# Kernel optimization log

Measured on AMD Instinct MI355X. Metric: run time of the kernel, lower is better.

The kernel has to match this reference:

```python
import jax, jax.numpy as jnp
import numpy as np

D = 1024      # hidden_size
FF = 4096     # ff_inner_dim = 4 * D
E = 8         # num_experts
K = 2         # moe_top_k
B, L = 4, 1024


def setup_inputs() -> dict:
    key = jax.random.key(0)
    ks = jax.random.split(key, 12)
    s = 0.02  # weight init scale
    return {
        "x": jax.random.normal(ks[0], (B, L, D), jnp.float32),
        "W_gate": jax.random.normal(ks[1], (D, E), jnp.float32) * s,
        "W1": jax.random.normal(ks[2], (E, D, FF), jnp.float32) * s,
        "b1": jnp.zeros((E, FF), jnp.float32),
        "W2": jax.random.normal(ks[3], (E, FF, D), jnp.float32) * s,
        "b2": jnp.zeros((E, D), jnp.float32),
        "Ws1": jax.random.normal(ks[4], (D, FF), jnp.float32) * s,
        "bs1": jnp.zeros((FF,), jnp.float32),
        "Ws2": jax.random.normal(ks[5], (FF, D), jnp.float32) * s,
        "bs2": jnp.zeros((D,), jnp.float32),
    }


def _gelu(h):
    # torch F.gelu default = exact (erf) gelu
    return jax.nn.gelu(h, approximate=False)


def reference(x, W_gate, W1, b1, W2, b2, Ws1, bs1, Ws2, bs2):
    Bx, Lx, Dx = x.shape
    xf = x.reshape(-1, Dx)                       # [T, D]
    logits = xf @ W_gate                         # [T, E]
    probs = jax.nn.softmax(logits, axis=-1)
    top_v, top_i = jax.lax.top_k(probs, K)       # [T, K]
    top_v = top_v / jnp.sum(top_v, axis=-1, keepdims=True)
    # dense combine weights: [T, E], zero for unselected experts
    combine = jnp.sum(jax.nn.one_hot(top_i, E, dtype=xf.dtype) * top_v[..., None], axis=1)

    out = jnp.zeros_like(xf)
    for e in range(E):  # fixed small expert loop, unrolled under jit
        h = _gelu(xf @ W1[e] + b1[e])            # [T, FF]
        out = out + combine[:, e:e + 1] * (h @ W2[e] + b2[e])

    shared = _gelu(xf @ Ws1 + bs1) @ Ws2 + bs2   # [T, D]
    return (out + shared).reshape(Bx, Lx, Dx)
```

## Files before the change

### kernel.cpp

```cpp
#include <hip/hip_runtime.h>
#include <hip/hip_bf16.h>

typedef unsigned short ushort_t;
typedef __attribute__((ext_vector_type(4))) float f32x4;
typedef __attribute__((ext_vector_type(8))) short bf16x8;
typedef __attribute__((ext_vector_type(8))) unsigned short us8;

#define T_TOK 4096
#define D_DIM 1024
#define FF_DIM 4096
#define NE 8
#define ESTRIDE 4194304L

__device__ __forceinline__ unsigned short f2bf(float f) {
  __hip_bfloat16 h = __float2bfloat16(f);
  return __builtin_bit_cast(unsigned short, h);
}
__device__ __forceinline__ float gelu_f(float v) {
  return 0.5f * v * (1.0f + erff(v * 0.70710678118654752440f));
}

__global__ void gate_kernel(const float* __restrict__ x, const float* __restrict__ Wg,
                            int* __restrict__ cnt, int* __restrict__ tok,
                            float* __restrict__ wof, int* __restrict__ rankof) {
  const int t = blockIdx.x;
  const int lane = threadIdx.x;
  const float* xr = x + (long)t * D_DIM;
  float acc[NE];
#pragma unroll
  for (int e = 0; e < NE; e++) acc[e] = 0.f;
#pragma unroll
  for (int i = 0; i < 16; i++) {
    int d = i * 64 + lane;
    float xv = xr[d];
    const float* wr = Wg + d * NE;
#pragma unroll
    for (int e = 0; e < NE; e++) acc[e] += xv * wr[e];
  }
#pragma unroll
  for (int off = 32; off > 0; off >>= 1) {
#pragma unroll
    for (int e = 0; e < NE; e++) acc[e] += __shfl_xor(acc[e], off, 64);
  }
  if (lane == 0) {
    int i0 = 0;
#pragma unroll
    for (int e = 1; e < NE; e++) if (acc[e] > acc[i0]) i0 = e;
    int i1 = -1;
#pragma unroll
    for (int e = 0; e < NE; e++) {
      if (e == i0) continue;
      if (i1 < 0 || acc[e] > acc[i1]) i1 = e;
    }
    float e1 = expf(acc[i1] - acc[i0]);
    float w0 = 1.f / (1.f + e1);
    float w1 = e1 * w0;
    int s0 = atomicAdd(&cnt[i0], 1);
    tok[i0 * T_TOK + s0] = t; wof[i0 * T_TOK + s0] = w0; rankof[i0 * T_TOK + s0] = 0;
    int s1 = atomicAdd(&cnt[i1], 1);
    tok[i1 * T_TOK + s1] = t; wof[i1 * T_TOK + s1] = w1; rankof[i1 * T_TOK + s1] = 1;
    tok[8 * T_TOK + t] = t; wof[8 * T_TOK + t] = 1.f; rankof[8 * T_TOK + t] = 0;
  }
}

__global__ void scan_kernel(int* cnt, int* base) {
  if (threadIdx.x == 0 && blockIdx.x == 0) {
    int s = 0;
    for (int e = 0; e < NE; e++) { base[e] = s; s += cnt[e]; }
    base[8] = s;
    cnt[8] = T_TOK;
  }
}

__global__ void cvt_x_kernel(const float* __restrict__ src, ushort_t* __restrict__ dst) {
  long i = ((long)blockIdx.x * 256 + threadIdx.x) * 8;
  float4 v0 = *(const float4*)(src + i);
  float4 v1 = *(const float4*)(src + i + 4);
  us8 o;
  o[0] = f2bf(v0.x); o[1] = f2bf(v0.y); o[2] = f2bf(v0.z); o[3] = f2bf(v0.w);
  o[4] = f2bf(v1.x); o[5] = f2bf(v1.y); o[6] = f2bf(v1.z); o[7] = f2bf(v1.w);
  *(us8*)(dst + i) = o;
}

__global__ void tcvt_kernel(const float* __restrict__ src, ushort_t* __restrict__ dst,
                            int R, int C) {
  src += (long)blockIdx.z * R * C;
  dst += (long)blockIdx.z * R * C;
  const int r0 = blockIdx.y * 64, c0 = blockIdx.x * 64;
  __shared__ ushort_t tile[64][72];
  const int t = threadIdx.x;
#pragma unroll
  for (int i = 0; i < 4; i++) {
    int lin = t + i * 256;
    int r = lin >> 4;
    int c = (lin & 15) * 4;
    float4 v = *(const float4*)(src + (long)(r0 + r) * C + c0 + c);
    tile[c + 0][r] = f2bf(v.x);
    tile[c + 1][r] = f2bf(v.y);
    tile[c + 2][r] = f2bf(v.z);
    tile[c + 3][r] = f2bf(v.w);
  }
  __syncthreads();
#pragma unroll
  for (int i = 0; i < 2; i++) {
    int lin = t + i * 256;
    int cc = lin >> 3, rp = lin & 7;
    us8 v = *(const us8*)&tile[cc][rp * 8];
    *(us8*)(dst + (long)(c0 + cc) * R + r0 + rp * 8) = v;
  }
}

template <int K, int N, int PHASE>
__global__ __launch_bounds__(512, 2) void gemm_kernel(
    const ushort_t* __restrict__ Abase, const ushort_t* __restrict__ WT,
    const float* __restrict__ bias_e, const float* __restrict__ bias_s,
    const int* __restrict__ cnt, const int* __restrict__ base,
    const int* __restrict__ tok, const float* __restrict__ wof,
    const int* __restrict__ rankof,
    ushort_t* __restrict__ He, float* __restrict__ ybuf, float* __restrict__ out) {
  const int e = blockIdx.z;
  const int count = cnt[e];
  const int m0 = blockIdx.y * 256;
  if (m0 >= count) return;
  const int n0 = blockIdx.x * 256;
  const int tid = threadIdx.x;
  const int w = tid >> 6, lane = tid & 63;
  const int wm = w >> 2, wn = w & 3;
  const int lr = lane & 15, lg = lane >> 4;

  __shared__ ushort_t lds_u[16 * 4096];
  char* const lds = (char*)lds_u;

  constexpr int NT = K / 32;

  const int srow = tid >> 2;
  const int kcg = (tid & 3) ^ ((tid >> 3) & 3);
  const ushort_t* bsrc[4];
#pragma unroll
  for (int c = 0; c < 2; c++) {
    int rr = m0 + c * 128 + srow;
    int rc = (rr < count) ? rr : 0;
    long arow;
    if (PHASE == 1) arow = tok[e * T_TOK + rc];
    else            arow = (long)base[e] + rc;
    bsrc[c] = Abase + arow * (long)K + kcg * 8;
  }
#pragma unroll
  for (int c = 0; c < 2; c++) {
    long brow = n0 + c * 128 + srow;
    bsrc[2 + c] = WT + (long)e * ESTRIDE + brow * (long)K + kcg * 8;
  }

#define STAGE(g_, c_, tg_)                                                     \
  __builtin_amdgcn_global_load_lds(                                            \
      (const __attribute__((address_space(1))) void*)(bsrc[c_] + (long)(tg_) * 32), \
      (__attribute__((address_space(3))) void*)(lds + ((g_) & 15) * 8192 + w * 1024), \
      16, 0, 0)

  int offA[8], offB[4];
#pragma unroll
  for (int m = 0; m < 8; m++) {
    int r = m * 16 + lr;
    offA[m] = r * 64 + ((lg ^ ((r >> 1) & 3)) << 4);
  }
#pragma unroll
  for (int n = 0; n < 4; n++) {
    int r = (wn & 1) * 64 + n * 16 + lr;
    offB[n] = r * 64 + ((lg ^ ((r >> 1) & 3)) << 4);
  }

  f32x4 acc[8][4] = {};

#pragma unroll
  for (int g = 0; g < 8; g++) STAGE(g, g & 3, g >> 2);

  int sA = wm;
  int sB = 2 + (wn >> 1);

  for (int t = 0; t < NT; t++) {
    if (t == NT - 1) { asm volatile("s_waitcnt vmcnt(0)" ::: "memory"); }
    else             { asm volatile("s_waitcnt vmcnt(4)" ::: "memory"); }
    __builtin_amdgcn_s_barrier();
    asm volatile("" ::: "memory");

    const char* pa = lds + sA * 8192;
    const char* pb = lds + sB * 8192;

    if (t + 2 < NT) { STAGE(4 * t + 8, 0, t + 2); STAGE(4 * t + 9, 1, t + 2); }
    bf16x8 av[8];
#pragma unroll
    for (int m = 0; m < 8; m++) av[m] = *(const bf16x8*)(pa + offA[m]);
    bf16x8 bv0 = *(const bf16x8*)(pb + offB[0]);
    bf16x8 bv1 = *(const bf16x8*)(pb + offB[1]);
    __builtin_amdgcn_s_setprio(1);
#pragma unroll
    for (int m = 0; m < 8; m++) {
      acc[m][0] = __builtin_amdgcn_mfma_f32_16x16x32_bf16(av[m], bv0, acc[m][0], 0, 0, 0);
      acc[m][1] = __builtin_amdgcn_mfma_f32_16x16x32_bf16(av[m], bv1, acc[m][1], 0, 0, 0);
    }
    __builtin_amdgcn_s_setprio(0);

    if (t + 2 < NT) { STAGE(4 * t + 10, 2, t + 2); STAGE(4 * t + 11, 3, t + 2); }
    bf16x8 bv2 = *(const bf16x8*)(pb + offB[2]);
    bf16x8 bv3 = *(const bf16x8*)(pb + offB[3]);
    __builtin_amdgcn_s_setprio(1);
#pragma unroll
    for (int m = 0; m < 8; m++) {
      acc[m][2] = __builtin_amdgcn_mfma_f32_16x16x32_bf16(av[m], bv2, acc[m][2], 0, 0, 0);
      acc[m][3] = __builtin_amdgcn_mfma_f32_16x16x32_bf16(av[m], bv3, acc[m][3], 0, 0, 0);
    }
    __builtin_amdgcn_s_setprio(0);

    sA = (sA + 4) & 15;
    sB = (sB + 4) & 15;
  }
#undef STAGE

  const float* bias = (e == NE) ? bias_s : (bias_e + (long)e * N);
#pragma unroll
  for (int m = 0; m < 8; m++) {
#pragma unroll
    for (int j = 0; j < 4; j++) {
      int rloc = wm * 128 + m * 16 + lg * 4 + j;
      int rr = m0 + rloc;
      if (rr >= count) continue;
      if (PHASE == 1) {
        long orow = (long)base[e] + rr;
#pragma unroll
        for (int n = 0; n < 4; n++) {
          int col = n0 + wn * 64 + n * 16 + lr;
          float v = acc[m][n][j] + bias[col];
          He[orow * FF_DIM + col] = f2bf(gelu_f(v));
        }
      } else {
        int tt = tok[e * T_TOK + rr];
        if (e == NE) {
#pragma unroll
          for (int n = 0; n < 4; n++) {
            int col = n0 + wn * 64 + n * 16 + lr;
            out[(long)tt * D_DIM + col] = acc[m][n][j] + bias[col];
          }
        } else {
          float wgt = wof[e * T_TOK + rr];
          int rk = rankof[e * T_TOK + rr];
          float* dst = ybuf + (long)rk * ((long)T_TOK * D_DIM) + (long)tt * D_DIM;
#pragma unroll
          for (int n = 0; n < 4; n++) {
            int col = n0 + wn * 64 + n * 16 + lr;
            dst[col] = wgt * (acc[m][n][j] + bias[col]);
          }
        }
      }
    }
  }
}

__global__ void final_add_kernel(float* __restrict__ out, const float* __restrict__ ybuf) {
  long i = ((long)blockIdx.x * 256 + threadIdx.x) * 4;
  float4 a = *(const float4*)(out + i);
  float4 b = *(const float4*)(ybuf + i);
  float4 c = *(const float4*)(ybuf + (long)T_TOK * D_DIM + i);
  a.x += b.x + c.x; a.y += b.y + c.y; a.z += b.z + c.z; a.w += b.w + c.w;
  *(float4*)(out + i) = a;
}

extern "C" void kernel_launch(void* const* d_in, const int* in_sizes, int n_in,
                              void* d_out, int out_size, void* d_ws, size_t ws_size,
                              hipStream_t stream) {
  (void)in_sizes; (void)n_in; (void)out_size; (void)ws_size;
  const float* x   = (const float*)d_in[0];
  const float* Wg  = (const float*)d_in[1];
  const float* W1  = (const float*)d_in[2];
  const float* b1  = (const float*)d_in[3];
  const float* W2  = (const float*)d_in[4];
  const float* b2  = (const float*)d_in[5];
  const float* Ws1 = (const float*)d_in[6];
  const float* bs1 = (const float*)d_in[7];
  const float* Ws2 = (const float*)d_in[8];
  const float* bs2 = (const float*)d_in[9];
  float* out = (float*)d_out;

  char* ws = (char*)d_ws;
  int*      cnt    = (int*)(ws + 0);
  int*      base   = (int*)(ws + 64);
  int*      tok    = (int*)(ws + 256);
  float*    wof    = (float*)(ws + 256 + 147456);
  int*      rankof = (int*)(ws + 256 + 2 * 147456);
  ushort_t* Xbf    = (ushort_t*)(ws + 442624);
  ushort_t* W1T    = (ushort_t*)(ws + 8831232);
  ushort_t* W2T    = (ushort_t*)(ws + 84328704);
  ushort_t* He     = (ushort_t*)(ws + 159826176);
  float*    ybuf   = (float*)(ws + 261538048);

  hipMemsetAsync(cnt, 0, 64, stream);
  gate_kernel<<<T_TOK, 64, 0, stream>>>(x, Wg, cnt, tok, wof, rankof);
  scan_kernel<<<1, 64, 0, stream>>>(cnt, base);
  cvt_x_kernel<<<2048, 256, 0, stream>>>(x, Xbf);
  tcvt_kernel<<<dim3(64, 16, 8), 256, 0, stream>>>(W1, W1T, 1024, 4096);
  tcvt_kernel<<<dim3(16, 64, 8), 256, 0, stream>>>(W2, W2T, 4096, 1024);
  tcvt_kernel<<<dim3(64, 16, 1), 256, 0, stream>>>(Ws1, W1T + 8L * ESTRIDE, 1024, 4096);
  tcvt_kernel<<<dim3(16, 64, 1), 256, 0, stream>>>(Ws2, W2T + 8L * ESTRIDE, 4096, 1024);
  gemm_kernel<1024, 4096, 1><<<dim3(16, 16, 9), 512, 0, stream>>>(
      Xbf, W1T, b1, bs1, cnt, base, tok, wof, rankof, He, ybuf, out);
  gemm_kernel<4096, 1024, 2><<<dim3(4, 16, 9), 512, 0, stream>>>(
      He, W2T, b2, bs2, cnt, base, tok, wof, rankof, He, ybuf, out);
  final_add_kernel<<<4096, 256, 0, stream>>>(out, ybuf);
}
```

Baseline: 627.3 us.

## Restructure MoE GEMM main loop into 4-phase ping-pong with K=64 tiles

New measurement: 625.9 us. Within noise of the previous version (-0.2%).

```diff
diff --git a/kernel.cpp b/kernel.cpp
--- a/kernel.cpp
+++ b/kernel.cpp
@@ -127,94 +127,141 @@
   const int w = tid >> 6, lane = tid & 63;
   const int wm = w >> 2, wn = w & 3;
   const int lr = lane & 15, lg = lane >> 4;
-
-  __shared__ ushort_t lds_u[16 * 4096];
+  const int swk = ((lg ^ ((lr >> 1) & 3)) << 4);
+
+  __shared__ ushort_t lds_u[2 * 32768];
   char* const lds = (char*)lds_u;
 
-  constexpr int NT = K / 32;
-
-  const int srow = tid >> 2;
-  const int kcg = (tid & 3) ^ ((tid >> 3) & 3);
-  const ushort_t* bsrc[4];
-#pragma unroll
-  for (int c = 0; c < 2; c++) {
-    int rr = m0 + c * 128 + srow;
+  constexpr int NT = K / 64;
+
+  const int sr2 = tid >> 2;
+  const int kc2 = (tid & 3) ^ ((tid >> 3) & 3);
+  const ushort_t* pA[2];
+  const ushort_t* pB[2];
+#pragma unroll
+  for (int h = 0; h < 2; h++) {
+    int rr = m0 + h * 128 + sr2;
     int rc = (rr < count) ? rr : 0;
     long arow;
     if (PHASE == 1) arow = tok[e * T_TOK + rc];
     else            arow = (long)base[e] + rc;
-    bsrc[c] = Abase + arow * (long)K + kcg * 8;
-  }
-#pragma unroll
-  for (int c = 0; c < 2; c++) {
-    long brow = n0 + c * 128 + srow;
-    bsrc[2 + c] = WT + (long)e * ESTRIDE + brow * (long)K + kcg * 8;
-  }
-
-#define STAGE(g_, c_, tg_)                                                     \
+    pA[h] = Abase + arow * (long)K + kc2 * 8;
+    pB[h] = WT + (long)e * ESTRIDE + (long)(n0 + h * 128 + sr2) * K + kc2 * 8;
+  }
+
+#define STG(p_, o_)                                                            \
   __builtin_amdgcn_global_load_lds(                                            \
-      (const __attribute__((address_space(1))) void*)(bsrc[c_] + (long)(tg_) * 32), \
-      (__attribute__((address_space(3))) void*)(lds + ((g_) & 15) * 8192 + w * 1024), \
-      16, 0, 0)
-
-  int offA[8], offB[4];
-#pragma unroll
-  for (int m = 0; m < 8; m++) {
-    int r = m * 16 + lr;
-    offA[m] = r * 64 + ((lg ^ ((r >> 1) & 3)) << 4);
-  }
-#pragma unroll
-  for (int n = 0; n < 4; n++) {
-    int r = (wn & 1) * 64 + n * 16 + lr;
-    offB[n] = r * 64 + ((lg ^ ((r >> 1) & 3)) << 4);
-  }
+      (const __attribute__((address_space(1))) void*)(p_),                     \
+      (__attribute__((address_space(3))) void*)(lds + (o_)), 16, 0, 0)
+#define STAGE_A(h_, kt_)                                                       \
+  do {                                                                         \
+    const ushort_t* s_ = pA[h_] + (long)(kt_) * 64;                            \
+    const int d_ = (((kt_) & 1) << 16) + ((h_) << 14) + (w << 10);             \
+    STG(s_, d_); STG(s_ + 32, d_ + 8192);                                      \
+  } while (0)
+#define STAGE_B(h_, kt_)                                                       \
+  do {                                                                         \
+    const ushort_t* s_ = pB[h_] + (long)(kt_) * 64;                            \
+    const int d_ = (((kt_) & 1) << 16) + 32768 + ((h_) << 14) + (w << 10);     \
+    STG(s_, d_); STG(s_ + 32, d_ + 8192);                                      \
+  } while (0)
+
+#define RD_A(mh_, mq_, kk_)                                                    \
+  (*(const bf16x8*)(aB + (kk_) * 8192 + ((mh_) * 64 + (mq_) * 16 + lr) * 64 + swk))
+#define RD_B(nh_, nq_, kk_)                                                    \
+  (*(const bf16x8*)(bB + (kk_) * 8192 +                                        \
+                    ((wn & 1) * 64 + (nh_) * 32 + (nq_) * 16 + lr) * 64 + swk))
+#define MFMA(a_, b_, c_) __builtin_amdgcn_mfma_f32_16x16x32_bf16(a_, b_, c_, 0, 0, 0)
 
   f32x4 acc[8][4] = {};
 
-#pragma unroll
-  for (int g = 0; g < 8; g++) STAGE(g, g & 3, g >> 2);
-
-  int sA = wm;
-  int sB = 2 + (wn >> 1);
+  STAGE_B(0, 0); STAGE_A(0, 0); STAGE_A(1, 0); STAGE_B(1, 0);
+  STAGE_B(0, 1); STAGE_A(0, 1);
+  asm volatile("s_waitcnt vmcnt(4)" ::: "memory");
+  __builtin_amdgcn_s_barrier();
+  asm volatile("" ::: "memory");
 
   for (int t = 0; t < NT; t++) {
-    if (t == NT - 1) { asm volatile("s_waitcnt vmcnt(0)" ::: "memory"); }
-    else             { asm volatile("s_waitcnt vmcnt(4)" ::: "memory"); }
+    const char* aB = lds + ((t & 1) << 16) + (wm << 14);
+    const char* bB = lds + ((t & 1) << 16) + 32768 + ((wn >> 1) << 14);
+    bf16x8 av[4][2], bvA[2][2], bvB[2][2];
+
+#pragma unroll
+    for (int mq = 0; mq < 4; mq++) { av[mq][0] = RD_A(0, mq, 0); av[mq][1] = RD_A(0, mq, 1); }
+#pragma unroll
+    for (int nq = 0; nq < 2; nq++) { bvA[nq][0] = RD_B(0, nq, 0); bvA[nq][1] = RD_B(0, nq, 1); }
+    if (t + 1 < NT) STAGE_A(1, t + 1);
+    __builtin_amdgcn_s_barrier();
+    asm volatile("s_waitcnt lgkmcnt(0)" ::: "memory");
+    __builtin_amdgcn_s_setprio(1);
+#pragma unroll
+    for (int mq = 0; mq < 4; mq++)
+#pragma unroll
+      for (int nq = 0; nq < 2; nq++) {
+        acc[mq][nq] = MFMA(av[mq][0], bvA[nq][0], acc[mq][nq]);
+        acc[mq][nq] = MFMA(av[mq][1], bvA[nq][1], acc[mq][nq]);
+      }
+    __builtin_amdgcn_s_setprio(0);
     __builtin_amdgcn_s_barrier();
     asm volatile("" ::: "memory");
 
-    const char* pa = lds + sA * 8192;
-    const char* pb = lds + sB * 8192;
-
-    if (t + 2 < NT) { STAGE(4 * t + 8, 0, t + 2); STAGE(4 * t + 9, 1, t + 2); }
-    bf16x8 av[8];
-#pragma unroll
-    for (int m = 0; m < 8; m++) av[m] = *(const bf16x8*)(pa + offA[m]);
-    bf16x8 bv0 = *(const bf16x8*)(pb + offB[0]);
-    bf16x8 bv1 = *(const bf16x8*)(pb + offB[1]);
+#pragma unroll
+    for (int nq = 0; nq < 2; nq++) { bvB[nq][0] = RD_B(1, nq, 0); bvB[nq][1] = RD_B(1, nq, 1); }
+    if (t + 1 < NT) STAGE_B(1, t + 1);
+    __builtin_amdgcn_s_barrier();
+    asm volatile("s_waitcnt lgkmcnt(0)" ::: "memory");
     __builtin_amdgcn_s_setprio(1);
 #pragma unroll
-    for (int m = 0; m < 8; m++) {
-      acc[m][0] = __builtin_amdgcn_mfma_f32_16x16x32_bf16(av[m], bv0, acc[m][0], 0, 0, 0);
-      acc[m][1] = __builtin_amdgcn_mfma_f32_16x16x32_bf16(av[m], bv1, acc[m][1], 0, 0, 0);
-    }
+    for (int mq = 0; mq < 4; mq++)
+#pragma unroll
+      for (int nq = 0; nq < 2; nq++) {
+        acc[mq][2 + nq] = MFMA(av[mq][0], bvB[nq][0], acc[mq][2 + nq]);
+        acc[mq][2 + nq] = MFMA(av[mq][1], bvB[nq][1], acc[mq][2 + nq]);
+      }
     __builtin_amdgcn_s_setprio(0);
-
-    if (t + 2 < NT) { STAGE(4 * t + 10, 2, t + 2); STAGE(4 * t + 11, 3, t + 2); }
-    bf16x8 bv2 = *(const bf16x8*)(pb + offB[2]);
-    bf16x8 bv3 = *(const bf16x8*)(pb + offB[3]);
+    __builtin_amdgcn_s_barrier();
+    asm volatile("" ::: "memory");
+
+#pragma unroll
+    for (int mq = 0; mq < 4; mq++) { av[mq][0] = RD_A(1, mq, 0); av[mq][1] = RD_A(1, mq, 1); }
+    if (t + 2 < NT) STAGE_B(0, t + 2);
+    __builtin_amdgcn_s_barrier();
+    asm volatile("s_waitcnt lgkmcnt(0)" ::: "memory");
     __builtin_amdgcn_s_setprio(1);
 #pragma unroll
-    for (int m = 0; m < 8; m++) {
-      acc[m][2] = __builtin_amdgcn_mfma_f32_16x16x32_bf16(av[m], bv2, acc[m][2], 0, 0, 0);
-      acc[m][3] = __builtin_amdgcn_mfma_f32_16x16x32_bf16(av[m], bv3, acc[m][3], 0, 0, 0);
-    }
+    for (int mq = 0; mq < 4; mq++)
+#pragma unroll
+      for (int nq = 0; nq < 2; nq++) {
+        acc[4 + mq][nq] = MFMA(av[mq][0], bvA[nq][0], acc[4 + mq][nq]);
+        acc[4 + mq][nq] = MFMA(av[mq][1], bvA[nq][1], acc[4 + mq][nq]);
+      }
     __builtin_amdgcn_s_setprio(0);
-
-    sA = (sA + 4) & 15;
-    sB = (sB + 4) & 15;
-  }
-#undef STAGE
+    __builtin_amdgcn_s_barrier();
+    asm volatile("" ::: "memory");
+
+    if (t + 2 < NT) STAGE_A(0, t + 2);
+    __builtin_amdgcn_s_barrier();
+    asm volatile("s_waitcnt lgkmcnt(0)" ::: "memory");
+    __builtin_amdgcn_s_setprio(1);
+#pragma unroll
+    for (int mq = 0; mq < 4; mq++)
+#pragma unroll
+      for (int nq = 0; nq < 2; nq++) {
+        acc[4 + mq][2 + nq] = MFMA(av[mq][0], bvB[nq][0], acc[4 + mq][2 + nq]);
+        acc[4 + mq][2 + nq] = MFMA(av[mq][1], bvB[nq][1], acc[4 + mq][2 + nq]);
+      }
+    __builtin_amdgcn_s_setprio(0);
+    if (t == NT - 2) asm volatile("s_waitcnt vmcnt(0)" ::: "memory");
+    else             asm volatile("s_waitcnt vmcnt(4)" ::: "memory");
+    __builtin_amdgcn_s_barrier();
+    asm volatile("" ::: "memory");
+  }
+#undef STG
+#undef STAGE_A
+#undef STAGE_B
+#undef RD_A
+#undef RD_B
+#undef MFMA
 
   const float* bias = (e == NE) ? bias_s : (bias_e + (long)e * N);
 #pragma unroll
```
